# Kernel optimization log

Measured on AMD Instinct MI355X. Metric: run time of the kernel, lower is better.

Reference implementation:

```python
import jax, jax.numpy as jnp
import numpy as np

N, C, E = 32768, 256, 16
LN_EPS = 1e-5
ENT_EPS = 1e-12


def setup_inputs() -> dict:
    key = jax.random.key(0)
    ks = jax.random.split(key, 8)
    return {
        "inputs": jax.random.normal(ks[0], (N, C), jnp.float32),
        "conv_out": jax.random.normal(ks[1], (N, C), jnp.float32),
        "domain_emb": jax.random.normal(ks[2], (C,), jnp.float32),
        "share_W": jax.random.normal(ks[3], (C, C), jnp.float32) * 0.02,
        "share_b": jnp.zeros((C,), jnp.float32),
        "gate_W": jax.random.normal(ks[4], (C, E), jnp.float32) * 0.1,
        "gate_b": jnp.zeros((E,), jnp.float32),
        "expert_W": jax.random.normal(ks[5], (E, C, C), jnp.float32) * 0.02,
        "expert_b": jnp.zeros((E, C), jnp.float32),
        "ln_gamma": jnp.ones((C,), jnp.float32),
        "ln_beta": jnp.zeros((C,), jnp.float32),
    }


def reference(inputs, conv_out, domain_emb, share_W, share_b, gate_W, gate_b,
              expert_W, expert_b, ln_gamma, ln_beta):
    n_exp = gate_W.shape[-1]

    # shared expert
    share_out = inputs @ share_W + share_b                      # (N, C)

    # LayerNorm on (stand-in) sparse-conv features + domain embedding
    mu = conv_out.mean(-1, keepdims=True)
    var = conv_out.var(-1, keepdims=True)
    route = (conv_out - mu) / jnp.sqrt(var + LN_EPS) * ln_gamma + ln_beta
    route = route + domain_emb                                   # (N, C)

    # router (eval path: no noise)
    gate_logits = route @ gate_W + gate_b                        # (N, E)
    w = jax.nn.softmax(gate_logits.astype(jnp.float32), axis=-1).astype(inputs.dtype)

    # entropy -> dynamic k per token
    entropy = -jnp.sum(w * jnp.log(w + ENT_EPS), axis=-1)        # (N,)
    max_entropy = jnp.log(jnp.float32(n_exp))
    k = jnp.ceil(1.0 + entropy / max_entropy * (n_exp - 1)).astype(jnp.int32)
    k = jnp.clip(k, 1, n_exp)                                    # (N,)

    # dynamic top-k selection mask (sort descending, keep first k)
    order = jnp.argsort(-w, axis=-1)                             # (N, E) descending ranks
    positions = jnp.arange(n_exp)[None, :]
    mask_sorted = positions < k[:, None]                         # (N, E) bool
    inv = jnp.argsort(order, axis=-1)                            # inverse permutation
    sel_mask = jnp.take_along_axis(mask_sorted, inv, axis=-1)    # (N, E) bool, expert-order
    combine = jnp.where(sel_mask, w, jnp.zeros_like(w))          # (N, E) combine weights

    # Switch-style load balancing loss
    frac_tokens = sel_mask.astype(jnp.float32).mean(0)           # (E,)
    frac_probs = w.astype(jnp.float32).mean(0)                   # (E,)
    loss_balance = jnp.mean(frac_tokens * frac_probs) * (n_exp ** 2)

    # expert compute + combine (dense, equivalent to gather/scatter loop)
    expert_out = jnp.einsum('nc,ecd->ned', inputs, expert_W) + expert_b  # (N, E, C)
    moe_out = jnp.einsum('ne,nec->nc', combine, expert_out)     # (N, C)

    return moe_out + share_out, loss_balance
```

## Files before the change

kernel.cpp:

```cpp
#include <hip/hip_runtime.h>
#include <hip/hip_bf16.h>

#define NTOK 32768
#define CH   256
#define NEXP 16

typedef __attribute__((ext_vector_type(8)))  short short8;
typedef __attribute__((ext_vector_type(16))) float f32x16;

#define MFMA32(a, b, c) __builtin_amdgcn_mfma_f32_32x32x16_bf16((a), (b), (c), 0, 0, 0)
#define BC8(v) __builtin_bit_cast(short8, (v))

#define GLD16(lds, g) __builtin_amdgcn_global_load_lds(                          \
    (const __attribute__((address_space(1))) unsigned int*)(g),                  \
    (__attribute__((address_space(3))) unsigned int*)(lds), 16, 0, 0)

static __device__ __forceinline__ unsigned short f2bf(float f) {
  unsigned int u = __builtin_bit_cast(unsigned int, f);
  unsigned int r = (u + 0x7fffu + ((u >> 16) & 1u)) >> 16;
  return (unsigned short)r;
}


__global__ __launch_bounds__(256) void wconvert_kernel(
    const float* __restrict__ share_W, const float* __restrict__ expert_W,
    uint4* __restrict__ wp) {
  int g = blockIdx.x * 256 + threadIdx.x;
  int e = g >> 13;
  int r = g & 8191;
  int lane = r & 63;
  int kb = (r >> 6) & 15;
  int db = r >> 10;
  int d  = db * 32 + (lane & 31);
  int k0 = kb * 16 + ((lane >> 5) << 3);
  const float* src = (e < 16) ? (expert_W + (size_t)e * 65536) : share_W;
  unsigned int p[4];
#pragma unroll
  for (int j = 0; j < 4; j++) {
    float f0 = src[(size_t)(k0 + 2 * j) * 256 + d];
    float f1 = src[(size_t)(k0 + 2 * j + 1) * 256 + d];
    p[j] = (unsigned int)f2bf(f0) | ((unsigned int)f2bf(f1) << 16);
  }
  wp[g] = make_uint4(p[0], p[1], p[2], p[3]);
}

__global__ __launch_bounds__(512, 2) void gate_kernel(
    const float* __restrict__ inputs, const float* __restrict__ conv_out,
    const float* __restrict__ domain_emb, const float* __restrict__ gate_W,
    const float* __restrict__ gate_b, const float* __restrict__ ln_gamma,
    const float* __restrict__ ln_beta, uint4* __restrict__ apack,
    float* __restrict__ combine, float* __restrict__ frac_part) {
  __shared__ __align__(16) unsigned short atile[64 * 256];
  __shared__ __align__(16) float gwT[16 * 260];
  __shared__ float route[8][256];
  __shared__ float fred[2][8][16];
  int t = threadIdx.x, b = blockIdx.x;
  int w = t >> 6, l = t & 63;

  for (int i = 0; i < 8; i++) {
    int idx = i * 512 + t;
    gwT[(idx & 15) * 260 + (idx >> 4)] = gate_W[idx];
  }

  for (int i = 0; i < 4; i++) {
    int idx = i * 512 + t;
    int row = idx >> 5;
    int j = idx & 31;
    const float4* src = (const float4*)(inputs + ((size_t)b * 64 + row) * 256 + j * 8);
    float4 f0 = src[0], f1 = src[1];
    unsigned int p0 = (unsigned int)f2bf(f0.x) | ((unsigned int)f2bf(f0.y) << 16);
    unsigned int p1 = (unsigned int)f2bf(f0.z) | ((unsigned int)f2bf(f0.w) << 16);
    unsigned int p2 = (unsigned int)f2bf(f1.x) | ((unsigned int)f2bf(f1.y) << 16);
    unsigned int p3 = (unsigned int)f2bf(f1.z) | ((unsigned int)f2bf(f1.w) << 16);
    int s = j ^ (row & 31);
    *(uint4*)(atile + (row * 32 + s) * 8) = make_uint4(p0, p1, p2, p3);
  }
  __syncthreads();
  for (int i = 0; i < 4; i++) {
    int L = i * 512 + t;
    int ll = L & 63;
    int mb = (L >> 6) & 1, kb = L >> 7;
    int row = mb * 32 + (ll & 31);
    int j = kb * 2 + (ll >> 5);
    int s = j ^ (row & 31);
    apack[(size_t)b * 2048 + L] = *(const uint4*)(atile + (row * 32 + s) * 8);
  }

  int lc = l * 4;
  float4 g4 = *(const float4*)(ln_gamma + lc);
  float4 be4 = *(const float4*)(ln_beta + lc);
  float4 de4 = *(const float4*)(domain_emb + lc);
  int e = l & 15, q = l >> 4;
  float gb = gate_b[e];
  float psel = 0.f, pw = 0.f;

  float4 gwreg[16];
#pragma unroll
  for (int ii = 0; ii < 16; ii++)
    gwreg[ii] = *(const float4*)&gwT[e * 260 + q * 64 + ii * 4];

  int n0 = b * 64 + w * 8;
  float4 x = *(const float4*)(conv_out + (size_t)n0 * 256 + lc);
  for (int i = 0; i < 8; i++) {
    float4 xn = *(const float4*)(conv_out + (size_t)(n0 + ((i + 1) & 7)) * 256 + lc);

    float s1 = x.x + x.y + x.z + x.w;
#pragma unroll
    for (int off = 1; off < 64; off <<= 1) s1 += __shfl_xor(s1, off);
    float mu = s1 * (1.f / 256.f);
    float dx = x.x - mu, dy = x.y - mu, dz = x.z - mu, dw = x.w - mu;
    float s2 = dx * dx + dy * dy + dz * dz + dw * dw;
#pragma unroll
    for (int off = 1; off < 64; off <<= 1) s2 += __shfl_xor(s2, off);
    float rstd = rsqrtf(s2 * (1.f / 256.f) + 1e-5f);
    float4 r;
    r.x = dx * rstd * g4.x + be4.x + de4.x;
    r.y = dy * rstd * g4.y + be4.y + de4.y;
    r.z = dz * rstd * g4.z + be4.z + de4.z;
    r.w = dw * rstd * g4.w + be4.w + de4.w;
    *(float4*)(&route[w][lc]) = r;
    asm volatile("s_waitcnt lgkmcnt(0)" ::: "memory");
    __builtin_amdgcn_wave_barrier();

    float a0 = 0.f, a1 = 0.f, a2 = 0.f, a3 = 0.f;
#pragma unroll
    for (int ii = 0; ii < 16; ii += 4) {
      float4 r0 = *(const float4*)(&route[w][q * 64 + (ii + 0) * 4]);
      float4 r1 = *(const float4*)(&route[w][q * 64 + (ii + 1) * 4]);
      float4 r2 = *(const float4*)(&route[w][q * 64 + (ii + 2) * 4]);
      float4 r3 = *(const float4*)(&route[w][q * 64 + (ii + 3) * 4]);
      a0 += r0.x * gwreg[ii + 0].x + r0.y * gwreg[ii + 0].y + r0.z * gwreg[ii + 0].z + r0.w * gwreg[ii + 0].w;
      a1 += r1.x * gwreg[ii + 1].x + r1.y * gwreg[ii + 1].y + r1.z * gwreg[ii + 1].z + r1.w * gwreg[ii + 1].w;
      a2 += r2.x * gwreg[ii + 2].x + r2.y * gwreg[ii + 2].y + r2.z * gwreg[ii + 2].z + r2.w * gwreg[ii + 2].w;
      a3 += r3.x * gwreg[ii + 3].x + r3.y * gwreg[ii + 3].y + r3.z * gwreg[ii + 3].z + r3.w * gwreg[ii + 3].w;
    }
    float acc = (a0 + a1) + (a2 + a3);
    acc += __shfl_xor(acc, 16);
    acc += __shfl_xor(acc, 32);
    float logit = acc + gb;

    float m = logit;
#pragma unroll
    for (int off = 1; off < 16; off <<= 1) m = fmaxf(m, __shfl_xor(m, off));
    float p = expf(logit - m);
    float sum = p;
#pragma unroll
    for (int off = 1; off < 16; off <<= 1) sum += __shfl_xor(sum, off);
    float wv = p / sum;

    float et = -wv * logf(wv + 1e-12f);
    float ent = et;
#pragma unroll
    for (int off = 1; off < 16; off <<= 1) ent += __shfl_xor(ent, off);
    float kf = ceilf(1.f + ent * (15.f / 2.7725887f));
    int k = (int)kf;
    k = max(1, min(16, k));

    int base = l & 48;
    int rank = 0;
#pragma unroll
    for (int j = 0; j < 16; j++) {
      float wj = __shfl(wv, base + j);
      rank += (wj > wv) || (wj == wv && j < e);
    }
    int sel = rank < k;
    float cmb = sel ? wv : 0.f;
    int n = n0 + i;
    if (l < 16) combine[(size_t)n * 16 + e] = cmb;
    psel += (float)sel;
    pw += wv;

    x = xn;
  }

  if (l < 16) { fred[0][w][l] = psel; fred[1][w][l] = pw; }
  __syncthreads();
  if (t < 32) {
    int kind = t >> 4, ee = t & 15;
    float v = 0.f;
#pragma unroll
    for (int ww = 0; ww < 8; ww++) v += fred[kind][ww][ee];
    frac_part[b * 32 + t] = v;
  }
}

static __device__ __forceinline__ void pref_b(
    uint4 (&breg)[8], const uint4* __restrict__ we, int q) {
#pragma unroll
  for (int f = 0; f < 8; f++) {
    int kbl = f >> 1, d = f & 1;
    breg[f] = we[(size_t)d * 1024 + (q * 4 + kbl) * 64];
  }
}

static __device__ __forceinline__ void slot_mfma(
    f32x16 (&tacc)[2][2], const f32x16& zc, const uint4* __restrict__ ab,
    const uint4 (&breg)[8], int q, bool first) {
  __builtin_amdgcn_s_setprio(1);
#pragma unroll
  for (int kbl = 0; kbl < 4; kbl++) {
    short8 a0 = BC8(ab[(q * 4 + kbl) * 256]);
    short8 a1 = BC8(ab[(q * 4 + kbl) * 256 + 64]);
    short8 b0 = BC8(breg[kbl * 2 + 0]);
    short8 b1 = BC8(breg[kbl * 2 + 1]);
    if (first && kbl == 0) {
      tacc[0][0] = MFMA32(a0, b0, zc);
      tacc[0][1] = MFMA32(a0, b1, zc);
      tacc[1][0] = MFMA32(a1, b0, zc);
      tacc[1][1] = MFMA32(a1, b1, zc);
    } else {
      tacc[0][0] = MFMA32(a0, b0, tacc[0][0]);
      tacc[0][1] = MFMA32(a0, b1, tacc[0][1]);
      tacc[1][0] = MFMA32(a1, b0, tacc[1][0]);
      tacc[1][1] = MFMA32(a1, b1, tacc[1][1]);
    }
  }
  __builtin_amdgcn_s_setprio(0);
}

__global__ __launch_bounds__(512, 2) void moe_gemm_kernel(
    const uint4* __restrict__ apack, const uint4* __restrict__ wpack,
    const float* __restrict__ combine, const float* __restrict__ expert_b,
    const float* __restrict__ share_b, float* __restrict__ out) {
  extern __shared__ __align__(16) char smem[];
  uint4* atile = (uint4*)smem;
  float* wtile = (float*)(smem + 65536);

  int t = threadIdx.x, b = blockIdx.x;
  int w = t >> 6, l = t & 63;
  int mbp = w >> 2;
  int dbp = w & 3;

#pragma unroll
  for (int i = 0; i < 8; i++) {
    int g = w * 8 + i;
    int kb = g >> 2, mb = g & 3;
    const uint4* src = apack + ((size_t)(2 * b + (mb >> 1)) * 2048 + (size_t)(kb * 2 + (mb & 1)) * 64 + l);
    GLD16(atile + g * 64, src);
  }
  {
    const float* cg = combine + (size_t)b * 2048;
#pragma unroll
    for (int i = 0; i < 4; i++) {
      int idx = i * 512 + t;
      wtile[(idx & 15) * 128 + (idx >> 4)] = cg[idx];
    }
  }
  __syncthreads();

  f32x16 facc[2][2];
#pragma unroll
  for (int mi = 0; mi < 2; mi++)
#pragma unroll
    for (int d = 0; d < 2; d++)
#pragma unroll
      for (int r = 0; r < 16; r++) facc[mi][d][r] = 0.f;
  f32x16 zc;
#pragma unroll
  for (int r = 0; r < 16; r++) zc[r] = 0.f;

  f32x16 tacc[2][2];
  int rowoff = (l >> 5) * 4;

  const uint4* ab = atile + (size_t)(mbp * 2) * 64 + l;
  const uint4* wb = wpack + (size_t)(dbp * 2) * 1024 + l;

  uint4 bregA[8], bregB[8];
  pref_b(bregA, wb, 0);

  for (int e = 0; e < 17; e++) {
    const uint4* we = wb + (size_t)e * 8192;
    pref_b(bregB, we, 1);
    slot_mfma(tacc, zc, ab, bregA, 0, true);
    pref_b(bregA, we, 2);
    slot_mfma(tacc, zc, ab, bregB, 1, false);
    pref_b(bregB, we, 3);
    slot_mfma(tacc, zc, ab, bregA, 2, false);
    if (e < 16) pref_b(bregA, we + 8192, 0);
    slot_mfma(tacc, zc, ab, bregB, 3, false);

    if (e < 16) {
#pragma unroll
      for (int mi = 0; mi < 2; mi++)
#pragma unroll
        for (int rg = 0; rg < 4; rg++) {
          float4 w4 = *(const float4*)&wtile[e * 128 + (mbp * 2 + mi) * 32 + 8 * rg + rowoff];
          float wj[4] = {w4.x, w4.y, w4.z, w4.w};
#pragma unroll
          for (int j = 0; j < 4; j++) {
            facc[mi][0][rg * 4 + j] += wj[j] * tacc[mi][0][rg * 4 + j];
            facc[mi][1][rg * 4 + j] += wj[j] * tacc[mi][1][rg * 4 + j];
          }
        }
    } else {
#pragma unroll
      for (int mi = 0; mi < 2; mi++)
#pragma unroll
        for (int r = 0; r < 16; r++) {
          facc[mi][0][r] += tacc[mi][0][r];
          facc[mi][1][r] += tacc[mi][1][r];
        }
    }
  }

  int col = l & 31;
  int cg0 = (dbp * 2 + 0) * 32 + col;
  int cg1 = (dbp * 2 + 1) * 32 + col;
  float sb0 = share_b[cg0], sb1 = share_b[cg1];
  float eb0[16], eb1[16];
#pragma unroll
  for (int e2 = 0; e2 < 16; e2++) {
    eb0[e2] = expert_b[e2 * 256 + cg0];
    eb1[e2] = expert_b[e2 * 256 + cg1];
  }
#pragma unroll
  for (int e2 = 0; e2 < 16; e2++)
#pragma unroll
    for (int mi = 0; mi < 2; mi++)
#pragma unroll
      for (int rg = 0; rg < 4; rg++) {
        float4 w4 = *(const float4*)&wtile[e2 * 128 + (mbp * 2 + mi) * 32 + 8 * rg + rowoff];
        float wj[4] = {w4.x, w4.y, w4.z, w4.w};
#pragma unroll
        for (int j = 0; j < 4; j++) {
          facc[mi][0][rg * 4 + j] += wj[j] * eb0[e2];
          facc[mi][1][rg * 4 + j] += wj[j] * eb1[e2];
        }
      }
#pragma unroll
  for (int mi = 0; mi < 2; mi++)
#pragma unroll
    for (int r = 0; r < 16; r++) {
      int row = (mbp * 2 + mi) * 32 + (r & 3) + ((r >> 2) << 3) + rowoff;
      size_t n = (size_t)b * 128 + row;
      out[n * 256 + cg0] = facc[mi][0][r] + sb0;
      out[n * 256 + cg1] = facc[mi][1][r] + sb1;
    }
}

__global__ __launch_bounds__(256) void finalize_kernel(
    const float* __restrict__ frac_part, float* __restrict__ loss_out) {
  __shared__ float acc[8][32];
  int t = threadIdx.x;
  int col = t & 31, seg = t >> 5;
  float s = 0.f;
  for (int i = seg; i < 512; i += 8) s += frac_part[i * 32 + col];
  acc[seg][col] = s;
  __syncthreads();
  if (t < 32) {
    float v = 0.f;
#pragma unroll
    for (int sg = 0; sg < 8; sg++) v += acc[sg][t];
    acc[0][t] = v;
  }
  __syncthreads();
  if (t == 0) {
    float loss = 0.f;
    for (int e = 0; e < 16; e++) {
      float ft = acc[0][e] * (1.f / 32768.f);
      float fp = acc[0][16 + e] * (1.f / 32768.f);
      loss += ft * fp;
    }
    loss_out[0] = loss * 16.f;
  }
}

extern "C" void kernel_launch(void* const* d_in, const int* in_sizes, int n_in,
                              void* d_out, int out_size, void* d_ws, size_t ws_size,
                              hipStream_t stream) {
  const float* inputs   = (const float*)d_in[0];
  const float* conv_out = (const float*)d_in[1];
  const float* demb     = (const float*)d_in[2];
  const float* share_W  = (const float*)d_in[3];
  const float* share_b  = (const float*)d_in[4];
  const float* gate_W   = (const float*)d_in[5];
  const float* gate_b   = (const float*)d_in[6];
  const float* expert_W = (const float*)d_in[7];
  const float* expert_b = (const float*)d_in[8];
  const float* ln_g     = (const float*)d_in[9];
  const float* ln_b     = (const float*)d_in[10];
  float* out = (float*)d_out;
  char* ws = (char*)d_ws;

  uint4* apack   = (uint4*)(ws);
  uint4* wpack   = (uint4*)(ws + 16777216);
  float* combine = (float*)(ws + 19005440);
  float* frac    = (float*)(ws + 21102592);

  hipFuncSetAttribute((const void*)moe_gemm_kernel,
                      hipFuncAttributeMaxDynamicSharedMemorySize, 73728);

  wconvert_kernel<<<dim3(544), dim3(256), 0, stream>>>(share_W, expert_W, wpack);
  gate_kernel<<<dim3(512), dim3(512), 0, stream>>>(inputs, conv_out, demb, gate_W,
                                                   gate_b, ln_g, ln_b, apack, combine, frac);
  moe_gemm_kernel<<<dim3(256), dim3(512), 73728, stream>>>(apack, wpack, combine,
                                                           expert_b, share_b, out);
  finalize_kernel<<<dim3(1), dim3(256), 0, stream>>>(frac, out + 8388608);
}
```

Measured before the change: 241.0 us.

## Merge weight conversion, gating and input packing into one prep kernel; fold finalize into GEMM

```diff
diff --git a/kernel.cpp b/kernel.cpp
--- a/kernel.cpp
+++ b/kernel.cpp
@@ -22,69 +22,76 @@
 }
 
 
-__global__ __launch_bounds__(256) void wconvert_kernel(
-    const float* __restrict__ share_W, const float* __restrict__ expert_W,
-    uint4* __restrict__ wp) {
-  int g = blockIdx.x * 256 + threadIdx.x;
-  int e = g >> 13;
-  int r = g & 8191;
-  int lane = r & 63;
-  int kb = (r >> 6) & 15;
-  int db = r >> 10;
-  int d  = db * 32 + (lane & 31);
-  int k0 = kb * 16 + ((lane >> 5) << 3);
-  const float* src = (e < 16) ? (expert_W + (size_t)e * 65536) : share_W;
-  unsigned int p[4];
-#pragma unroll
-  for (int j = 0; j < 4; j++) {
-    float f0 = src[(size_t)(k0 + 2 * j) * 256 + d];
-    float f1 = src[(size_t)(k0 + 2 * j + 1) * 256 + d];
-    p[j] = (unsigned int)f2bf(f0) | ((unsigned int)f2bf(f1) << 16);
-  }
-  wp[g] = make_uint4(p[0], p[1], p[2], p[3]);
-}
-
-__global__ __launch_bounds__(512, 2) void gate_kernel(
+__global__ __launch_bounds__(512, 2) void prep_kernel(
     const float* __restrict__ inputs, const float* __restrict__ conv_out,
     const float* __restrict__ domain_emb, const float* __restrict__ gate_W,
     const float* __restrict__ gate_b, const float* __restrict__ ln_gamma,
-    const float* __restrict__ ln_beta, uint4* __restrict__ apack,
-    float* __restrict__ combine, float* __restrict__ frac_part) {
-  __shared__ __align__(16) unsigned short atile[64 * 256];
-  __shared__ __align__(16) float gwT[16 * 260];
-  __shared__ float route[8][256];
-  __shared__ float fred[2][8][16];
+    const float* __restrict__ ln_beta, const float* __restrict__ share_W,
+    const float* __restrict__ expert_W, float* __restrict__ combine,
+    float* __restrict__ frac_part, uint4* __restrict__ wp,
+    uint4* __restrict__ apack) {
+  __shared__ __align__(16) char shm[33280];
   int t = threadIdx.x, b = blockIdx.x;
+
+  if (b >= 784) {
+    uint4* at = (uint4*)shm;
+    int tile = b - 784;
+#pragma unroll
+    for (int i = 0; i < 4; i++) {
+      int u = i * 512 + t;
+      int row = u >> 5, j = u & 31;
+      const float4* src = (const float4*)(inputs + ((size_t)tile * 64 + row) * 256 + j * 8);
+      float4 f0 = src[0], f1 = src[1];
+      unsigned int p0 = (unsigned int)f2bf(f0.x) | ((unsigned int)f2bf(f0.y) << 16);
+      unsigned int p1 = (unsigned int)f2bf(f0.z) | ((unsigned int)f2bf(f0.w) << 16);
+      unsigned int p2 = (unsigned int)f2bf(f1.x) | ((unsigned int)f2bf(f1.y) << 16);
+      unsigned int p3 = (unsigned int)f2bf(f1.z) | ((unsigned int)f2bf(f1.w) << 16);
+      int kb = j >> 1, hib = j & 1;
+      at[kb * 128 + (row >> 5) * 64 + hib * 32 + ((row & 31) ^ kb)] =
+          make_uint4(p0, p1, p2, p3);
+    }
+    __syncthreads();
+#pragma unroll
+    for (int i = 0; i < 4; i++) {
+      int u = i * 512 + t;
+      int kb = u >> 7, mb = (u >> 6) & 1, hib = (u >> 5) & 1, r5 = u & 31;
+      apack[(size_t)tile * 2048 + u] = at[kb * 128 + mb * 64 + hib * 32 + (r5 ^ kb)];
+    }
+    return;
+  }
+
+  if (b >= 512) {
+    int g = (b - 512) * 512 + t;
+    int e = g >> 13;
+    int r = g & 8191;
+    int lane = r & 63;
+    int kb = (r >> 6) & 15;
+    int db = r >> 10;
+    int d  = db * 32 + (lane & 31);
+    int k0 = kb * 16 + ((lane >> 5) << 3);
+    const float* src = (e < 16) ? (expert_W + (size_t)e * 65536) : share_W;
+    unsigned int p[4];
+#pragma unroll
+    for (int j = 0; j < 4; j++) {
+      float f0 = src[(size_t)(k0 + 2 * j) * 256 + d];
+      float f1 = src[(size_t)(k0 + 2 * j + 1) * 256 + d];
+      p[j] = (unsigned int)f2bf(f0) | ((unsigned int)f2bf(f1) << 16);
+    }
+    wp[g] = make_uint4(p[0], p[1], p[2], p[3]);
+    return;
+  }
+
+  float (*route)[256] = (float(*)[256])shm;
+  float* gwT = (float*)(shm + 8192);
+  float* fred = (float*)(shm + 8192 + 16640);
   int w = t >> 6, l = t & 63;
 
+#pragma unroll
   for (int i = 0; i < 8; i++) {
     int idx = i * 512 + t;
     gwT[(idx & 15) * 260 + (idx >> 4)] = gate_W[idx];
   }
-
-  for (int i = 0; i < 4; i++) {
-    int idx = i * 512 + t;
-    int row = idx >> 5;
-    int j = idx & 31;
-    const float4* src = (const float4*)(inputs + ((size_t)b * 64 + row) * 256 + j * 8);
-    float4 f0 = src[0], f1 = src[1];
-    unsigned int p0 = (unsigned int)f2bf(f0.x) | ((unsigned int)f2bf(f0.y) << 16);
-    unsigned int p1 = (unsigned int)f2bf(f0.z) | ((unsigned int)f2bf(f0.w) << 16);
-    unsigned int p2 = (unsigned int)f2bf(f1.x) | ((unsigned int)f2bf(f1.y) << 16);
-    unsigned int p3 = (unsigned int)f2bf(f1.z) | ((unsigned int)f2bf(f1.w) << 16);
-    int s = j ^ (row & 31);
-    *(uint4*)(atile + (row * 32 + s) * 8) = make_uint4(p0, p1, p2, p3);
-  }
   __syncthreads();
-  for (int i = 0; i < 4; i++) {
-    int L = i * 512 + t;
-    int ll = L & 63;
-    int mb = (L >> 6) & 1, kb = L >> 7;
-    int row = mb * 32 + (ll & 31);
-    int j = kb * 2 + (ll >> 5);
-    int s = j ^ (row & 31);
-    apack[(size_t)b * 2048 + L] = *(const uint4*)(atile + (row * 32 + s) * 8);
-  }
 
   int lc = l * 4;
   float4 g4 = *(const float4*)(ln_gamma + lc);
@@ -92,13 +99,13 @@
   float4 de4 = *(const float4*)(domain_emb + lc);
   int e = l & 15, q = l >> 4;
   float gb = gate_b[e];
-  float psel = 0.f, pw = 0.f;
 
   float4 gwreg[16];
 #pragma unroll
   for (int ii = 0; ii < 16; ii++)
     gwreg[ii] = *(const float4*)&gwT[e * 260 + q * 64 + ii * 4];
 
+  float psel = 0.f, pw = 0.f;
   int n0 = b * 64 + w * 8;
   float4 x = *(const float4*)(conv_out + (size_t)n0 * 256 + lc);
   for (int i = 0; i < 8; i++) {
@@ -173,13 +180,13 @@
     x = xn;
   }
 
-  if (l < 16) { fred[0][w][l] = psel; fred[1][w][l] = pw; }
+  if (l < 16) { fred[0 * 128 + w * 16 + l] = psel; fred[1 * 128 + w * 16 + l] = pw; }
   __syncthreads();
   if (t < 32) {
     int kind = t >> 4, ee = t & 15;
     float v = 0.f;
 #pragma unroll
-    for (int ww = 0; ww < 8; ww++) v += fred[kind][ww][ee];
+    for (int ww = 0; ww < 8; ww++) v += fred[kind * 128 + ww * 16 + ee];
     frac_part[b * 32 + t] = v;
   }
 }
@@ -194,13 +201,17 @@
 }
 
 static __device__ __forceinline__ void slot_mfma(
-    f32x16 (&tacc)[2][2], const f32x16& zc, const uint4* __restrict__ ab,
-    const uint4 (&breg)[8], int q, bool first) {
+    f32x16 (&tacc)[2][2], const f32x16& zc, const uint4* __restrict__ at,
+    const uint4 (&breg)[8], int q, int abase_kb_stride_l, int mbp, int l,
+    bool first) {
+  (void)abase_kb_stride_l;
   __builtin_amdgcn_s_setprio(1);
 #pragma unroll
   for (int kbl = 0; kbl < 4; kbl++) {
-    short8 a0 = BC8(ab[(q * 4 + kbl) * 256]);
-    short8 a1 = BC8(ab[(q * 4 + kbl) * 256 + 64]);
+    int g0 = ((q * 4 + kbl) * 4 + (mbp * 2 + 0)) * 64 + l;
+    int g1 = ((q * 4 + kbl) * 4 + (mbp * 2 + 1)) * 64 + l;
+    short8 a0 = BC8(at[g0]);
+    short8 a1 = BC8(at[g1]);
     short8 b0 = BC8(breg[kbl * 2 + 0]);
     short8 b1 = BC8(breg[kbl * 2 + 1]);
     if (first && kbl == 0) {
@@ -221,12 +232,40 @@
 __global__ __launch_bounds__(512, 2) void moe_gemm_kernel(
     const uint4* __restrict__ apack, const uint4* __restrict__ wpack,
     const float* __restrict__ combine, const float* __restrict__ expert_b,
-    const float* __restrict__ share_b, float* __restrict__ out) {
+    const float* __restrict__ share_b, float* __restrict__ out,
+    const float* __restrict__ frac_part) {
   extern __shared__ __align__(16) char smem[];
+  int t = threadIdx.x, b = blockIdx.x;
+
+  if (b == 256) {
+    float* acc = (float*)smem;
+    int col = t & 31, seg = t >> 5;
+    float s = 0.f;
+    for (int i = seg; i < 512; i += 16) s += frac_part[i * 32 + col];
+    acc[seg * 32 + col] = s;
+    __syncthreads();
+    if (t < 32) {
+      float v = 0.f;
+#pragma unroll
+      for (int sg = 0; sg < 16; sg++) v += acc[sg * 32 + t];
+      acc[t] = v;
+    }
+    __syncthreads();
+    if (t == 0) {
+      float loss = 0.f;
+      for (int e = 0; e < 16; e++) {
+        float ft = acc[e] * (1.f / 32768.f);
+        float fp = acc[16 + e] * (1.f / 32768.f);
+        loss += ft * fp;
+      }
+      out[8388608] = loss * 16.f;
+    }
+    return;
+  }
+
   uint4* atile = (uint4*)smem;
   float* wtile = (float*)(smem + 65536);
 
-  int t = threadIdx.x, b = blockIdx.x;
   int w = t >> 6, l = t & 63;
   int mbp = w >> 2;
   int dbp = w & 3;
@@ -246,6 +285,11 @@
       wtile[(idx & 15) * 128 + (idx >> 4)] = cg[idx];
     }
   }
+
+  const uint4* wb = wpack + (size_t)(dbp * 2) * 1024 + l;
+  uint4 bregA[8], bregB[8];
+  pref_b(bregA, wb, 0);
+
   __syncthreads();
 
   f32x16 facc[2][2];
@@ -261,23 +305,17 @@
 
   f32x16 tacc[2][2];
   int rowoff = (l >> 5) * 4;
-
-  const uint4* ab = atile + (size_t)(mbp * 2) * 64 + l;
-  const uint4* wb = wpack + (size_t)(dbp * 2) * 1024 + l;
-
-  uint4 bregA[8], bregB[8];
-  pref_b(bregA, wb, 0);
 
   for (int e = 0; e < 17; e++) {
     const uint4* we = wb + (size_t)e * 8192;
     pref_b(bregB, we, 1);
-    slot_mfma(tacc, zc, ab, bregA, 0, true);
+    slot_mfma(tacc, zc, atile, bregA, 0, 0, mbp, l, true);
     pref_b(bregA, we, 2);
-    slot_mfma(tacc, zc, ab, bregB, 1, false);
+    slot_mfma(tacc, zc, atile, bregB, 1, 0, mbp, l, false);
     pref_b(bregB, we, 3);
-    slot_mfma(tacc, zc, ab, bregA, 2, false);
+    slot_mfma(tacc, zc, atile, bregA, 2, 0, mbp, l, false);
     if (e < 16) pref_b(bregA, we + 8192, 0);
-    slot_mfma(tacc, zc, ab, bregB, 3, false);
+    slot_mfma(tacc, zc, atile, bregB, 3, 0, mbp, l, false);
 
     if (e < 16) {
 #pragma unroll
@@ -336,33 +374,6 @@
       out[n * 256 + cg0] = facc[mi][0][r] + sb0;
       out[n * 256 + cg1] = facc[mi][1][r] + sb1;
     }
-}
-
-__global__ __launch_bounds__(256) void finalize_kernel(
-    const float* __restrict__ frac_part, float* __restrict__ loss_out) {
-  __shared__ float acc[8][32];
-  int t = threadIdx.x;
-  int col = t & 31, seg = t >> 5;
-  float s = 0.f;
-  for (int i = seg; i < 512; i += 8) s += frac_part[i * 32 + col];
-  acc[seg][col] = s;
-  __syncthreads();
-  if (t < 32) {
-    float v = 0.f;
-#pragma unroll
-    for (int sg = 0; sg < 8; sg++) v += acc[sg][t];
-    acc[0][t] = v;
-  }
-  __syncthreads();
-  if (t == 0) {
-    float loss = 0.f;
-    for (int e = 0; e < 16; e++) {
-      float ft = acc[0][e] * (1.f / 32768.f);
-      float fp = acc[0][16 + e] * (1.f / 32768.f);
-      loss += ft * fp;
-    }
-    loss_out[0] = loss * 16.f;
-  }
 }
 
 extern "C" void kernel_launch(void* const* d_in, const int* in_sizes, int n_in,
@@ -382,18 +393,17 @@
   float* out = (float*)d_out;
   char* ws = (char*)d_ws;
 
-  uint4* apack   = (uint4*)(ws);
-  uint4* wpack   = (uint4*)(ws + 16777216);
+  uint4* wpack   = (uint4*)(ws);
+  uint4* apack   = (uint4*)(ws + 2228224);
   float* combine = (float*)(ws + 19005440);
   float* frac    = (float*)(ws + 21102592);
 
   hipFuncSetAttribute((const void*)moe_gemm_kernel,
                       hipFuncAttributeMaxDynamicSharedMemorySize, 73728);
 
-  wconvert_kernel<<<dim3(544), dim3(256), 0, stream>>>(share_W, expert_W, wpack);
-  gate_kernel<<<dim3(512), dim3(512), 0, stream>>>(inputs, conv_out, demb, gate_W,
-                                                   gate_b, ln_g, ln_b, apack, combine, frac);
-  moe_gemm_kernel<<<dim3(256), dim3(512), 73728, stream>>>(apack, wpack, combine,
-                                                           expert_b, share_b, out);
-  finalize_kernel<<<dim3(1), dim3(256), 0, stream>>>(frac, out + 8388608);
-}
+  prep_kernel<<<dim3(1296), dim3(512), 0, stream>>>(
+      inputs, conv_out, demb, gate_W, gate_b, ln_g, ln_b, share_W, expert_W,
+      combine, frac, wpack, apack);
+  moe_gemm_kernel<<<dim3(257), dim3(512), 73728, stream>>>(
+      apack, wpack, combine, expert_b, share_b, out, frac);
+}
```

Result: faster. 227.6 us (-5.6%).
